# Kernel tuning notes

Measured on AMD Instinct MI355X. Metric: run time of the kernel, lower is better.

Reference implementation:

```python
import jax, jax.numpy as jnp
import numpy as np

B, IN_DIM, OUT_DIM, HID, K, GH, NG = 512, 480, 400, 512, 8, 128, 32


def setup_inputs() -> dict:
    key = jax.random.key(0)
    ks = jax.random.split(key, 8)
    s = lambda fan: 1.0 / np.sqrt(fan)
    return {
        "x": jax.random.normal(ks[0], (B, IN_DIM), jnp.float32),
        "gating_idx": jnp.arange(NG, dtype=jnp.int64) + (IN_DIM - NG),
        "GW1": jax.random.normal(ks[1], (NG, GH), jnp.float32) * s(NG),
        "Gb1": jnp.zeros((GH,), jnp.float32),
        "GW2": jax.random.normal(ks[2], (GH, GH), jnp.float32) * s(GH),
        "Gb2": jnp.zeros((GH,), jnp.float32),
        "GW3": jax.random.normal(ks[3], (GH, K), jnp.float32) * s(GH),
        "Gb3": jnp.zeros((K,), jnp.float32),
        "Wk1": jax.random.normal(ks[4], (K, HID, IN_DIM), jnp.float32) * s(HID * IN_DIM) * 2.45,
        "bk1": jnp.zeros((K, HID), jnp.float32),
        "Wk2": jax.random.normal(ks[5], (K, HID, HID), jnp.float32) * s(HID * HID) * 2.45,
        "bk2": jnp.zeros((K, HID), jnp.float32),
        "Wk3": jax.random.normal(ks[6], (K, OUT_DIM, HID), jnp.float32) * s(OUT_DIM * HID) * 2.45,
        "bk3": jnp.zeros((K, OUT_DIM), jnp.float32),
    }


def _motion_layer(xin, g, Wk, bk):
    # blended per-sample weight: wi[b,o,i] = sum_k g[b,k] * Wk[k,o,i]
    # then per-sample matvec: out[b,o] = sum_i wi[b,o,i] * xin[b,i] + sum_k g[b,k]*bk[k,o]
    out = jnp.einsum('bk,koi,bi->bo', g, Wk, xin)
    return out + g @ bk


def reference(x, gating_idx, GW1, Gb1, GW2, Gb2, GW3, Gb3,
              Wk1, bk1, Wk2, bk2, Wk3, bk3):
    # gating MLP (elu, elu, linear)
    g_in = jnp.take(x, gating_idx, axis=-1)                 # [B, NG]
    h = jax.nn.elu(g_in @ GW1 + Gb1)
    h = jax.nn.elu(h @ GW2 + Gb2)
    g = h @ GW3 + Gb3                                       # [B, K] blend coefficients
    # motion network: 3 phase-blended expert layers
    y1 = jax.nn.elu(_motion_layer(x, g, Wk1, bk1))          # [B, HID]
    y2 = jax.nn.elu(_motion_layer(y1, g, Wk2, bk2))         # [B, HID]
    out = _motion_layer(y2, g, Wk3, bk3)                    # [B, OUT_DIM]
    return out
```

## Files before the change

### kernel.cpp

```cpp
#include <hip/hip_runtime.h>
#include <hip/hip_bf16.h>


typedef __hip_bfloat16 bf16;
typedef unsigned short u16;
typedef __attribute__((ext_vector_type(8))) short bf16x8;
typedef __attribute__((ext_vector_type(4))) float f32x4;

__device__ __forceinline__ float elu1(float x) { return x > 0.f ? x : expm1f(x); }

__device__ __forceinline__ short cvt1(float v) {
    union { bf16 h; u16 u; } c;
    c.h = __float2bfloat16(v);
    return (short)c.u;
}

__global__ __launch_bounds__(128) void gating_xcvt_kernel(
    const float* __restrict__ x, const int* __restrict__ idx_raw,
    const float* __restrict__ GW1, const float* __restrict__ Gb1,
    const float* __restrict__ GW2, const float* __restrict__ Gb2,
    const float* __restrict__ GW3, const float* __restrict__ Gb3,
    float* __restrict__ g, u16* __restrict__ xbf)
{
    __shared__ float xg[32];
    __shared__ float h1[128];
    __shared__ float h2[128];
    const int b = blockIdx.x;
    const int j = threadIdx.x;

    for (int i = j; i < 480; i += 128)
        xbf[b * 480 + i] = (u16)cvt1(x[b * 480 + i]);

    if (j < 32) {
        int ii;
        if (idx_raw[1] == 0) ii = (int)((const long long*)idx_raw)[j];
        else                 ii = idx_raw[j];
        if (ii < 0 || ii >= 480) ii = 448 + j;
        xg[j] = x[(size_t)b * 480 + ii];
    }
    __syncthreads();

    float a = Gb1[j];
    #pragma unroll
    for (int i = 0; i < 32; ++i) a += xg[i] * GW1[i * 128 + j];
    h1[j] = elu1(a);
    __syncthreads();

    float a2 = Gb2[j];
    #pragma unroll 8
    for (int i = 0; i < 128; ++i) a2 += h1[i] * GW2[i * 128 + j];
    h2[j] = elu1(a2);
    __syncthreads();

    if (j < 8) {
        float a3 = Gb3[j];
        for (int i = 0; i < 128; ++i) a3 += h2[i] * GW3[i * 8 + j];
        g[b * 8 + j] = a3;
    }
}

template <int IDIM, int ODIM, bool ELU, typename OutT>
__global__ __launch_bounds__(256) void layer_kernel(
    const u16*  __restrict__ A,
    const float* __restrict__ W,
    const float* __restrict__ bk,
    const float* __restrict__ g,
    OutT* __restrict__ out)
{
    constexpr int KW = 128;
    constexpr int NW = (IDIM + KW - 1) / KW;
    __shared__ u16 wbuf[2][8 * 16 * KW];

    const int ot = blockIdx.x & 31;
    const int o0 = ot * 16;
    if (o0 >= ODIM) return;
    const int m0  = (blockIdx.x >> 5) * 64;
    const int tid  = threadIdx.x;
    const int wid  = tid >> 6;
    const int lane = tid & 63;
    const int n    = lane & 15;
    const int quad = lane >> 4;
    const int e0   = wid * 2;

    float4 lv[16];
    auto load_units = [&](int w) {
        const int w0 = w * KW;
        #pragma unroll
        for (int jj = 0; jj < 8; ++jj) {
            const int u = tid + 256 * jj;
            const int r = u >> 4, c = u & 15;
            const int e = r >> 4, nr = r & 15;
            if (w0 + c * 8 + 8 <= IDIM) {
                const float* p = W + ((size_t)(e * ODIM + o0 + nr)) * IDIM + w0 + c * 8;
                lv[2 * jj]     = *(const float4*)p;
                lv[2 * jj + 1] = *(const float4*)(p + 4);
            } else {
                lv[2 * jj]     = float4{0.f, 0.f, 0.f, 0.f};
                lv[2 * jj + 1] = float4{0.f, 0.f, 0.f, 0.f};
            }
        }
    };
    auto write_units = [&](u16* buf) {
        #pragma unroll
        for (int jj = 0; jj < 8; ++jj) {
            const int u = tid + 256 * jj;
            const int r = u >> 4, c = u & 15;
            const int nr = r & 15;
            bf16x8 hv;
            hv[0] = cvt1(lv[2 * jj].x);     hv[1] = cvt1(lv[2 * jj].y);
            hv[2] = cvt1(lv[2 * jj].z);     hv[3] = cvt1(lv[2 * jj].w);
            hv[4] = cvt1(lv[2 * jj + 1].x); hv[5] = cvt1(lv[2 * jj + 1].y);
            hv[6] = cvt1(lv[2 * jj + 1].z); hv[7] = cvt1(lv[2 * jj + 1].w);
            *(bf16x8*)(buf + r * KW + ((c ^ (nr & 7)) << 3)) = hv;
        }
    };

    const f32x4 zero = {0.f, 0.f, 0.f, 0.f};
    f32x4 acc[4][2] = {{zero, zero}, {zero, zero}, {zero, zero}, {zero, zero}};

    load_units(0);
    write_units(wbuf[0]);
    __syncthreads();

    for (int w = 0; w < NW; ++w) {
        if (w + 1 < NW) load_units(w + 1);

        const u16* buf = wbuf[w & 1];
        #pragma unroll
        for (int cl = 0; cl < KW / 32; ++cl) {
            const int i0 = w * KW + cl * 32;
            if (i0 >= IDIM) break;
            bf16x8 af[4];
            #pragma unroll
            for (int s = 0; s < 4; ++s)
                af[s] = *(const bf16x8*)(A + (size_t)(m0 + 16 * s + n) * IDIM
                                           + i0 + quad * 8);
            const int cw = cl * 4 + quad;
            #pragma unroll
            for (int e = 0; e < 2; ++e) {
                bf16x8 bfr = *(const bf16x8*)(buf + ((e0 + e) * 16 + n) * KW
                                                  + ((cw ^ (n & 7)) << 3));
                #pragma unroll
                for (int s = 0; s < 4; ++s)
                    acc[s][e] = __builtin_amdgcn_mfma_f32_16x16x32_bf16(
                                    af[s], bfr, acc[s][e], 0, 0, 0);
            }
        }

        if (w + 1 < NW) write_units(wbuf[(w + 1) & 1]);
        __syncthreads();
    }

    const float bk0 = bk[e0 * ODIM + o0 + n];
    const float bk1 = bk[(e0 + 1) * ODIM + o0 + n];
    float* part = (float*)wbuf;
    #pragma unroll
    for (int s = 0; s < 4; ++s) {
        f32x4 v;
        #pragma unroll
        for (int r = 0; r < 4; ++r) {
            const int row = m0 + 16 * s + quad * 4 + r;
            const float gA = g[row * 8 + e0];
            const float gB = g[row * 8 + e0 + 1];
            v[r] = gA * (acc[s][0][r] + bk0) + gB * (acc[s][1][r] + bk1);
        }
        *(f32x4*)(part + (wid * 16 + n) * 68 + 16 * s + quad * 4) = v;
    }
    __syncthreads();

    f32x4 t = zero;
    #pragma unroll
    for (int w4 = 0; w4 < 4; ++w4)
        t += *(const f32x4*)(part + (w4 * 16 + n) * 68 + 16 * wid + quad * 4);
    #pragma unroll
    for (int r = 0; r < 4; ++r) {
        float val = t[r];
        if (ELU) val = elu1(val);
        const int row = m0 + 16 * wid + quad * 4 + r;
        if constexpr (__hip_internal::is_same<OutT, float>::value)
            out[(size_t)row * ODIM + o0 + n] = val;
        else
            out[(size_t)row * ODIM + o0 + n] = (OutT)cvt1(val);
    }
}

extern "C" void kernel_launch(void* const* d_in, const int* in_sizes, int n_in,
                              void* d_out, int out_size, void* d_ws, size_t ws_size,
                              hipStream_t stream)
{
    const float* x   = (const float*)d_in[0];
    const int* gidx  = (const int*)d_in[1];
    const float* GW1 = (const float*)d_in[2];
    const float* Gb1 = (const float*)d_in[3];
    const float* GW2 = (const float*)d_in[4];
    const float* Gb2 = (const float*)d_in[5];
    const float* GW3 = (const float*)d_in[6];
    const float* Gb3 = (const float*)d_in[7];
    const float* Wk1 = (const float*)d_in[8];
    const float* bk1 = (const float*)d_in[9];
    const float* Wk2 = (const float*)d_in[10];
    const float* bk2 = (const float*)d_in[11];
    const float* Wk3 = (const float*)d_in[12];
    const float* bk3 = (const float*)d_in[13];

    char* ws  = (char*)d_ws;
    float* g  = (float*)ws;
    u16*  xbf = (u16*)(ws + (16 << 10));
    u16*  A1  = (u16*)(ws + (1 << 20));
    u16*  A2  = (u16*)(ws + (1 << 20) + (512 << 10));

    gating_xcvt_kernel<<<512, 128, 0, stream>>>(x, gidx, GW1, Gb1, GW2, Gb2,
                                                GW3, Gb3, g, xbf);

    layer_kernel<480, 512, true,  u16>  <<<256, 256, 0, stream>>>(xbf, Wk1, bk1, g, A1);
    layer_kernel<512, 512, true,  u16>  <<<256, 256, 0, stream>>>(A1,  Wk2, bk2, g, A2);
    layer_kernel<512, 400, false, float><<<256, 256, 0, stream>>>(A2,  Wk3, bk3, g,
                                                                  (float*)d_out);
}
```

Measured before the change: 140.5 us.

## Pre-convert expert weights to bf16 in gating kernel and rebalance warp tiling

The gating kernel now also converts all three expert weight tensors to bf16 in workspace, so layer kernels load half-size bf16 tiles without per-tile conversion. Warps are re-split into 2 row-tiles by 4 experts, changing the cross-warp reduction to two halves. This trades an extra full-weight write and read pass for reduced redundant fp32 traffic and conversion across batch tiles.

Result: slower. 149.5 us (+6.4%).

```diff
diff --git a/kernel.cpp b/kernel.cpp
--- a/kernel.cpp
+++ b/kernel.cpp
@@ -9,18 +9,21 @@
 
 __device__ __forceinline__ float elu1(float x) { return x > 0.f ? x : expm1f(x); }
 
-__device__ __forceinline__ short cvt1(float v) {
+__device__ __forceinline__ u16 cvt1(float v) {
     union { bf16 h; u16 u; } c;
     c.h = __float2bfloat16(v);
-    return (short)c.u;
-}
-
-__global__ __launch_bounds__(128) void gating_xcvt_kernel(
+    return c.u;
+}
+
+__global__ __launch_bounds__(256) void gating_cvt_kernel(
     const float* __restrict__ x, const int* __restrict__ idx_raw,
     const float* __restrict__ GW1, const float* __restrict__ Gb1,
     const float* __restrict__ GW2, const float* __restrict__ Gb2,
     const float* __restrict__ GW3, const float* __restrict__ Gb3,
-    float* __restrict__ g, u16* __restrict__ xbf)
+    const float* __restrict__ Wk1, const float* __restrict__ Wk2,
+    const float* __restrict__ Wk3,
+    float* __restrict__ g, u16* __restrict__ xbf,
+    u16* __restrict__ Wb1, u16* __restrict__ Wb2, u16* __restrict__ Wb3)
 {
     __shared__ float xg[32];
     __shared__ float h1[128];
@@ -28,9 +31,6 @@
     const int b = blockIdx.x;
     const int j = threadIdx.x;
 
-    for (int i = j; i < 480; i += 128)
-        xbf[b * 480 + i] = (u16)cvt1(x[b * 480 + i]);
-
     if (j < 32) {
         int ii;
         if (idx_raw[1] == 0) ii = (int)((const long long*)idx_raw)[j];
@@ -40,16 +40,20 @@
     }
     __syncthreads();
 
-    float a = Gb1[j];
-    #pragma unroll
-    for (int i = 0; i < 32; ++i) a += xg[i] * GW1[i * 128 + j];
-    h1[j] = elu1(a);
-    __syncthreads();
-
-    float a2 = Gb2[j];
-    #pragma unroll 8
-    for (int i = 0; i < 128; ++i) a2 += h1[i] * GW2[i * 128 + j];
-    h2[j] = elu1(a2);
+    if (j < 128) {
+        float a = Gb1[j];
+        #pragma unroll
+        for (int i = 0; i < 32; ++i) a += xg[i] * GW1[i * 128 + j];
+        h1[j] = elu1(a);
+    }
+    __syncthreads();
+
+    if (j < 128) {
+        float a2 = Gb2[j];
+        #pragma unroll 8
+        for (int i = 0; i < 128; ++i) a2 += h1[i] * GW2[i * 128 + j];
+        h2[j] = elu1(a2);
+    }
     __syncthreads();
 
     if (j < 8) {
@@ -57,32 +61,54 @@
         for (int i = 0; i < 128; ++i) a3 += h2[i] * GW3[i * 8 + j];
         g[b * 8 + j] = a3;
     }
+
+    for (int i = j; i < 480; i += 256)
+        xbf[b * 480 + i] = cvt1(x[b * 480 + i]);
+
+    #pragma unroll
+    for (int jj = 0; jj < 6; ++jj) {
+        const int local = jj * 256 + j;
+        if (local >= 1392) break;
+        const int u = b * 1392 + local;
+        const float* src; u16* dst; size_t off;
+        if (u < 245760)      { src = Wk1; dst = Wb1; off = (size_t)u * 8; }
+        else if (u < 507904) { src = Wk2; dst = Wb2; off = (size_t)(u - 245760) * 8; }
+        else                 { src = Wk3; dst = Wb3; off = (size_t)(u - 507904) * 8; }
+        float4 a = *(const float4*)(src + off);
+        float4 c = *(const float4*)(src + off + 4);
+        union { u16 h[8]; uint4 v; } o;
+        o.h[0] = cvt1(a.x); o.h[1] = cvt1(a.y); o.h[2] = cvt1(a.z); o.h[3] = cvt1(a.w);
+        o.h[4] = cvt1(c.x); o.h[5] = cvt1(c.y); o.h[6] = cvt1(c.z); o.h[7] = cvt1(c.w);
+        *(uint4*)(dst + off) = o.v;
+    }
 }
 
 template <int IDIM, int ODIM, bool ELU, typename OutT>
 __global__ __launch_bounds__(256) void layer_kernel(
     const u16*  __restrict__ A,
-    const float* __restrict__ W,
+    const u16*  __restrict__ Wb,
     const float* __restrict__ bk,
     const float* __restrict__ g,
     OutT* __restrict__ out)
 {
     constexpr int KW = 128;
     constexpr int NW = (IDIM + KW - 1) / KW;
-    __shared__ u16 wbuf[2][8 * 16 * KW];
+    __shared__ u16 wbuf[2][128 * KW];
 
     const int ot = blockIdx.x & 31;
     const int o0 = ot * 16;
     if (o0 >= ODIM) return;
-    const int m0  = (blockIdx.x >> 5) * 64;
+    const int m0   = (blockIdx.x >> 5) * 64;
     const int tid  = threadIdx.x;
     const int wid  = tid >> 6;
     const int lane = tid & 63;
     const int n    = lane & 15;
     const int quad = lane >> 4;
-    const int e0   = wid * 2;
-
-    float4 lv[16];
+    const int w_m  = wid & 1;
+    const int w_e  = wid >> 1;
+    const int e0   = w_e * 4;
+
+    uint4 lv[8];
     auto load_units = [&](int w) {
         const int w0 = w * KW;
         #pragma unroll
@@ -90,14 +116,11 @@
             const int u = tid + 256 * jj;
             const int r = u >> 4, c = u & 15;
             const int e = r >> 4, nr = r & 15;
-            if (w0 + c * 8 + 8 <= IDIM) {
-                const float* p = W + ((size_t)(e * ODIM + o0 + nr)) * IDIM + w0 + c * 8;
-                lv[2 * jj]     = *(const float4*)p;
-                lv[2 * jj + 1] = *(const float4*)(p + 4);
-            } else {
-                lv[2 * jj]     = float4{0.f, 0.f, 0.f, 0.f};
-                lv[2 * jj + 1] = float4{0.f, 0.f, 0.f, 0.f};
-            }
+            if (w0 + c * 8 + 8 <= IDIM)
+                lv[jj] = *(const uint4*)(Wb + ((size_t)(e * ODIM + o0 + nr)) * IDIM
+                                            + w0 + c * 8);
+            else
+                lv[jj] = uint4{0u, 0u, 0u, 0u};
         }
     };
     auto write_units = [&](u16* buf) {
@@ -106,17 +129,12 @@
             const int u = tid + 256 * jj;
             const int r = u >> 4, c = u & 15;
             const int nr = r & 15;
-            bf16x8 hv;
-            hv[0] = cvt1(lv[2 * jj].x);     hv[1] = cvt1(lv[2 * jj].y);
-            hv[2] = cvt1(lv[2 * jj].z);     hv[3] = cvt1(lv[2 * jj].w);
-            hv[4] = cvt1(lv[2 * jj + 1].x); hv[5] = cvt1(lv[2 * jj + 1].y);
-            hv[6] = cvt1(lv[2 * jj + 1].z); hv[7] = cvt1(lv[2 * jj + 1].w);
-            *(bf16x8*)(buf + r * KW + ((c ^ (nr & 7)) << 3)) = hv;
+            *(uint4*)(buf + r * KW + ((c ^ (nr & 7)) << 3)) = lv[jj];
         }
     };
 
     const f32x4 zero = {0.f, 0.f, 0.f, 0.f};
-    f32x4 acc[4][2] = {{zero, zero}, {zero, zero}, {zero, zero}, {zero, zero}};
+    f32x4 acc[2][4] = {{zero, zero, zero, zero}, {zero, zero, zero, zero}};
 
     load_units(0);
     write_units(wbuf[0]);
@@ -130,20 +148,18 @@
         for (int cl = 0; cl < KW / 32; ++cl) {
             const int i0 = w * KW + cl * 32;
             if (i0 >= IDIM) break;
-            bf16x8 af[4];
+            bf16x8 af[2];
             #pragma unroll
-            for (int s = 0; s < 4; ++s)
-                af[s] = *(const bf16x8*)(A + (size_t)(m0 + 16 * s + n) * IDIM
+            for (int s = 0; s < 2; ++s)
+                af[s] = *(const bf16x8*)(A + (size_t)(m0 + 16 * (2 * w_m + s) + n) * IDIM
                                            + i0 + quad * 8);
             const int cw = cl * 4 + quad;
             #pragma unroll
-            for (int e = 0; e < 2; ++e) {
-                bf16x8 bfr = *(const bf16x8*)(buf + ((e0 + e) * 16 + n) * KW
+            for (int j = 0; j < 4; ++j) {
+                bf16x8 bfr = *(const bf16x8*)(buf + ((e0 + j) * 16 + n) * KW
                                                   + ((cw ^ (n & 7)) << 3));
-                #pragma unroll
-                for (int s = 0; s < 4; ++s)
-                    acc[s][e] = __builtin_amdgcn_mfma_f32_16x16x32_bf16(
-                                    af[s], bfr, acc[s][e], 0, 0, 0);
+                acc[0][j] = __builtin_amdgcn_mfma_f32_16x16x32_bf16(af[0], bfr, acc[0][j], 0, 0, 0);
+                acc[1][j] = __builtin_amdgcn_mfma_f32_16x16x32_bf16(af[1], bfr, acc[1][j], 0, 0, 0);
             }
         }
 
@@ -151,36 +167,36 @@
         __syncthreads();
     }
 
-    const float bk0 = bk[e0 * ODIM + o0 + n];
-    const float bk1 = bk[(e0 + 1) * ODIM + o0 + n];
     float* part = (float*)wbuf;
-    #pragma unroll
-    for (int s = 0; s < 4; ++s) {
-        f32x4 v;
+    float bkv[4];
+    #pragma unroll
+    for (int j = 0; j < 4; ++j) bkv[j] = bk[(e0 + j) * ODIM + o0 + n];
+
+    #pragma unroll
+    for (int s = 0; s < 2; ++s) {
         #pragma unroll
         for (int r = 0; r < 4; ++r) {
-            const int row = m0 + 16 * s + quad * 4 + r;
-            const float gA = g[row * 8 + e0];
-            const float gB = g[row * 8 + e0 + 1];
-            v[r] = gA * (acc[s][0][r] + bk0) + gB * (acc[s][1][r] + bk1);
-        }
-        *(f32x4*)(part + (wid * 16 + n) * 68 + 16 * s + quad * 4) = v;
-    }
-    __syncthreads();
-
-    f32x4 t = zero;
-    #pragma unroll
-    for (int w4 = 0; w4 < 4; ++w4)
-        t += *(const f32x4*)(part + (w4 * 16 + n) * 68 + 16 * wid + quad * 4);
-    #pragma unroll
-    for (int r = 0; r < 4; ++r) {
-        float val = t[r];
-        if (ELU) val = elu1(val);
-        const int row = m0 + 16 * wid + quad * 4 + r;
+            const int lrow = 16 * (2 * w_m + s) + 4 * quad + r;
+            const int grow = m0 + lrow;
+            float v = 0.f;
+            #pragma unroll
+            for (int j = 0; j < 4; ++j)
+                v += g[grow * 8 + e0 + j] * (acc[s][j][r] + bkv[j]);
+            part[(w_e * 64 + lrow) * 17 + n] = v;
+        }
+    }
+    __syncthreads();
+
+    #pragma unroll
+    for (int rr = 0; rr < 4; ++rr) {
+        const int lrow = 16 * wid + 4 * quad + rr;
+        float v = part[lrow * 17 + n] + part[(64 + lrow) * 17 + n];
+        if (ELU) v = elu1(v);
+        const int grow = m0 + lrow;
         if constexpr (__hip_internal::is_same<OutT, float>::value)
-            out[(size_t)row * ODIM + o0 + n] = val;
+            out[(size_t)grow * ODIM + o0 + n] = v;
         else
-            out[(size_t)row * ODIM + o0 + n] = (OutT)cvt1(val);
+            out[(size_t)grow * ODIM + o0 + n] = cvt1(v);
     }
 }
 
@@ -205,15 +221,19 @@
 
     char* ws  = (char*)d_ws;
     float* g  = (float*)ws;
-    u16*  xbf = (u16*)(ws + (16 << 10));
-    u16*  A1  = (u16*)(ws + (1 << 20));
-    u16*  A2  = (u16*)(ws + (1 << 20) + (512 << 10));
-
-    gating_xcvt_kernel<<<512, 128, 0, stream>>>(x, gidx, GW1, Gb1, GW2, Gb2,
-                                                GW3, Gb3, g, xbf);
-
-    layer_kernel<480, 512, true,  u16>  <<<256, 256, 0, stream>>>(xbf, Wk1, bk1, g, A1);
-    layer_kernel<512, 512, true,  u16>  <<<256, 256, 0, stream>>>(A1,  Wk2, bk2, g, A2);
-    layer_kernel<512, 400, false, float><<<256, 256, 0, stream>>>(A2,  Wk3, bk3, g,
+    u16* xbf  = (u16*)(ws + (64 << 10));
+    u16* A1   = (u16*)(ws + (1 << 20));
+    u16* A2   = (u16*)(ws + (1 << 20) + (512 << 10));
+    u16* Wb1  = (u16*)(ws + (2 << 20));
+    u16* Wb2  = (u16*)(ws + (6 << 20));
+    u16* Wb3  = (u16*)(ws + (10 << 20));
+
+    gating_cvt_kernel<<<512, 256, 0, stream>>>(x, gidx, GW1, Gb1, GW2, Gb2,
+                                               GW3, Gb3, Wk1, Wk2, Wk3,
+                                               g, xbf, Wb1, Wb2, Wb3);
+
+    layer_kernel<480, 512, true,  u16>  <<<256, 256, 0, stream>>>(xbf, Wb1, bk1, g, A1);
+    layer_kernel<512, 512, true,  u16>  <<<256, 256, 0, stream>>>(A1,  Wb2, bk2, g, A2);
+    layer_kernel<512, 400, false, float><<<256, 256, 0, stream>>>(A2,  Wb3, bk3, g,
                                                                   (float*)d_out);
 }
```
